# Optimization experiments

Hardware: AMD Instinct MI355X
Metric: run time of the kernel (lower is better)

## Reference

```python
import jax, jax.numpy as jnp
import numpy as np

B, N, D, H = 2, 2048, 1024, 16
DH = D // H            # 64
PH = 3 * DH            # 192 per-head proj dim (module quirk: 3*Dh per head)
P = H * PH             # 3072 total projection width


def setup_inputs() -> dict:
    key = jax.random.key(0)
    ks = jax.random.split(key, 8)
    s = 0.02
    return {
        "input": jax.random.normal(ks[0], (B, N, D), dtype=jnp.float32),
        "q_w": jax.random.normal(ks[1], (D, P), dtype=jnp.float32) * s,
        "q_b": jnp.zeros((P,), dtype=jnp.float32),
        "k_w": jax.random.normal(ks[2], (D, P), dtype=jnp.float32) * s,
        "k_b": jnp.zeros((P,), dtype=jnp.float32),
        "v_w": jax.random.normal(ks[3], (D, P), dtype=jnp.float32) * s,
        "v_b": jnp.zeros((P,), dtype=jnp.float32),
        "o_w": jax.random.normal(ks[4], (P, D), dtype=jnp.float32) * s,
        "o_b": jnp.zeros((D,), dtype=jnp.float32),
    }


def reference(input, q_w, q_b, k_w, k_b, v_w, v_b, o_w, o_b):
    def heads(y):  # [B,N,H*PH] -> [B,H,N,PH]
        return y.reshape(B, N, H, PH).transpose(0, 2, 1, 3)

    q_mat = heads(input @ q_w + q_b)
    # faithful to source: v_mat uses the 'k' projection, k_mat uses the 'v' projection
    v_mat = heads(input @ k_w + k_b)
    k_mat = heads(input @ v_w + v_b)

    scale = 1.0 / jnp.sqrt(jnp.float32(DH * H))  # sqrt(dim), per source
    scores = jnp.einsum('bhnd,bhmd->bhnm', q_mat, k_mat) * scale
    weights = jax.nn.softmax(scores, axis=-1)
    inter = jnp.einsum('bhnm,bhmd->bhnd', weights, v_mat)
    inter = inter.transpose(0, 2, 1, 3).reshape(B, N, P)  # b n (h d)
    return inter @ o_w + o_b
```

## Files before the change

### kernel.cpp

```cpp
#include <hip/hip_runtime.h>
#include <cstdint>
#include <cstddef>

typedef __bf16 bf16;
typedef __attribute__((ext_vector_type(8))) __bf16 bf16x8;
typedef __attribute__((ext_vector_type(4))) __bf16 bf16x4;
typedef __attribute__((ext_vector_type(2))) __bf16 bf16x2;
typedef __attribute__((ext_vector_type(4))) float f32x4;

#define MFMA_16x16x32(a, b, c) __builtin_amdgcn_mfma_f32_16x16x32_bf16((a), (b), (c), 0, 0, 0)

#define VMCNT(N) asm volatile("s_waitcnt vmcnt(" #N ")" ::: "memory")
#define LGK0                                           \
  {                                                    \
    asm volatile("s_waitcnt lgkmcnt(0)" ::: "memory"); \
    __builtin_amdgcn_sched_barrier(0);                 \
  }

__device__ __forceinline__ void gload_lds16(const void* g, void* l) {
  __builtin_amdgcn_global_load_lds((__attribute__((address_space(1))) void*)g,
                                   (__attribute__((address_space(3))) void*)l,
                                   16, 0, 0);
}

__global__ __launch_bounds__(256) void prep_kernel(const float* __restrict__ X,
                                                   const float* __restrict__ q_w,
                                                   const float* __restrict__ v_w,
                                                   const float* __restrict__ k_w,
                                                   const float* __restrict__ o_w,
                                                   bf16* __restrict__ Xb,
                                                   bf16* __restrict__ Wqkv,
                                                   bf16* __restrict__ Wot) {
  __shared__ float tile[32][33];
  int blk = blockIdx.x;
  if (blk < 4096) {
    int i = blk * 256 + threadIdx.x;
    float4 v = ((const float4*)X)[i];
    bf16x4 o = {(bf16)v.x, (bf16)v.y, (bf16)v.z, (bf16)v.w};
    ((bf16x4*)Xb)[i] = o;
    return;
  }
  const float* in;
  bf16* out;
  int R, C, t;
  if (blk < 13312) {
    t = blk - 4096;
    int widx = t / 3072;
    t -= widx * 3072;
    in = widx == 0 ? q_w : (widx == 1 ? v_w : k_w);
    out = Wqkv + (size_t)widx * 3072 * 1024;
    R = 1024;
    C = 3072;
  } else {
    t = blk - 13312;
    in = o_w;
    out = Wot;
    R = 3072;
    C = 1024;
  }
  int tiles_c = C >> 5;
  int br = t / tiles_c, bc = t % tiles_c;
  int r0 = br << 5, c0 = bc << 5;
  int tr = threadIdx.x >> 5, tc = threadIdx.x & 31;
#pragma unroll
  for (int i = 0; i < 4; i++)
    tile[tr + 8 * i][tc] = in[(size_t)(r0 + tr + 8 * i) * C + c0 + tc];
  __syncthreads();
#pragma unroll
  for (int i = 0; i < 4; i++) {
    int oc = tr + 8 * i;
    out[(size_t)(c0 + oc) * R + r0 + tc] = (bf16)tile[tc][oc];
  }
}

__global__ __launch_bounds__(512, 2) void gemm_fused_qkv(
    const bf16* __restrict__ A, const bf16* __restrict__ Bt,
    const float* __restrict__ q_b, const float* __restrict__ v_b,
    const float* __restrict__ k_b,
    bf16* __restrict__ Qm, bf16* __restrict__ Km, bf16* __restrict__ Vt) {
  constexpr int K = 1024, NT = 16;
  __shared__ __align__(16) bf16 sA[2][2][128 * 32];
  __shared__ __align__(16) bf16 sB[2][192 * 64];

  int bid = blockIdx.x;
  int xcd = bid & 7, j = bid >> 3;
  int bm = xcd * 4 + (j & 3), bn = j >> 2;
  int m0 = bm << 7, n0 = bn * 192;

  int tid = threadIdx.x, lane = tid & 63, w = tid >> 6;
  int wr = w >> 2, wc = w & 3;
  int l15 = lane & 15, lg = lane >> 4;

  int sra = lane >> 2, sca = lane & 3;
  const bf16* gA = A + (size_t)(m0 + w * 16 + sra) * K + ((sca ^ ((sra >> 1) & 3)) * 8);
  int srb = lane >> 3, scb = lane & 7;
  const bf16* gB = Bt + (size_t)(n0 + w * 24 + srb) * K + ((scb ^ srb) * 8);

#define STAGE_AB(BUF, T)                                                   \
  {                                                                        \
    _Pragma("unroll") for (int kh = 0; kh < 2; kh++)                       \
        gload_lds16(gA + (size_t)(T) * 64 + kh * 32, &sA[BUF][kh][w * 512]); \
    _Pragma("unroll") for (int ii = 0; ii < 3; ii++)                       \
        gload_lds16(gB + (size_t)(ii * 8) * K + (T) * 64,                  \
                    &sB[BUF][(w * 3 + ii) * 512]);                         \
  }

  int slotA = lg ^ ((l15 >> 1) & 3);
  int aBase = wr * 2048 + l15 * 32 + slotA * 8;
  int bBase = (wc * 48 + l15) * 64;
  int sB0 = (lg ^ (l15 & 7)) * 8;
  int sB1 = ((4 + lg) ^ (l15 & 7)) * 8;

#define RD_A(BUF, KH)                                                      \
  _Pragma("unroll") for (int mf = 0; mf < 4; mf++)                         \
      a[mf] = *(const bf16x8*)&sA[BUF][KH][aBase + mf * 512];
#define RD_B(BUF, SLOT)                                                    \
  _Pragma("unroll") for (int nf = 0; nf < 3; nf++)                         \
      b[nf] = *(const bf16x8*)&sB[BUF][bBase + nf * 1024 + (SLOT)];
#define MFMA12                                                             \
  _Pragma("unroll") for (int mf = 0; mf < 4; mf++)                         \
      _Pragma("unroll") for (int nf = 0; nf < 3; nf++)                     \
          acc[mf][nf] = MFMA_16x16x32(a[mf], b[nf], acc[mf][nf]);

  f32x4 acc[4][3];
#pragma unroll
  for (int mf = 0; mf < 4; mf++)
#pragma unroll
    for (int nf = 0; nf < 3; nf++) acc[mf][nf] = (f32x4){0.f, 0.f, 0.f, 0.f};

  STAGE_AB(0, 0);

#pragma unroll 2
  for (int s = 0; s < NT; s++) {
    int buf = s & 1, nbuf = buf ^ 1;
    int nxt = (s + 1) & (NT - 1);
    bf16x8 a[4], b[3];

    STAGE_AB(nbuf, nxt);
    VMCNT(5);
    __builtin_amdgcn_s_barrier();

    RD_A(buf, 0);
    RD_B(buf, sB0);
    LGK0;
    __builtin_amdgcn_s_setprio(1);
    MFMA12;
    __builtin_amdgcn_s_setprio(0);

    RD_A(buf, 1);
    RD_B(buf, sB1);
    LGK0;
    __builtin_amdgcn_s_barrier();
    __builtin_amdgcn_s_setprio(1);
    MFMA12;
    __builtin_amdgcn_s_setprio(0);
  }

  int seg = bn >> 4;
  int segbn = bn & 15;
  const float* bias = seg == 0 ? q_b : (seg == 1 ? v_b : k_b);
  bf16* outQK = seg == 0 ? Qm : Km;
#pragma unroll
  for (int mf = 0; mf < 4; mf++) {
#pragma unroll
    for (int nf = 0; nf < 3; nf++) {
      int colL = segbn * 192 + wc * 48 + nf * 16 + l15;
      int row0 = m0 + wr * 64 + mf * 16 + lg * 4;
      float bv = bias[colL];
      if (seg < 2) {
#pragma unroll
        for (int r = 0; r < 4; r++)
          outQK[(size_t)(row0 + r) * 3072 + colL] = (bf16)(acc[mf][nf][r] + bv);
      } else {
        int hh = colL / 192, dd = colL % 192;
        int bi = row0 >> 11, nn = row0 & 2047;
        bf16x4 pk = {(bf16)(acc[mf][nf][0] + bv), (bf16)(acc[mf][nf][1] + bv),
                     (bf16)(acc[mf][nf][2] + bv), (bf16)(acc[mf][nf][3] + bv)};
        *(bf16x4*)(Vt + (((size_t)bi * 16 + hh) * 192 + dd) * 2048 + nn) = pk;
      }
    }
  }
#undef STAGE_AB
#undef RD_A
#undef RD_B
#undef MFMA12
}

__global__ __launch_bounds__(256, 3) void gemm_oproj(const bf16* __restrict__ A,
                                                     const bf16* __restrict__ Bt,
                                                     const float* __restrict__ bias,
                                                     float* __restrict__ out) {
  constexpr int K = 3072, NT = 48;
  __shared__ __align__(16) bf16 sA[2][2][128 * 32];
  __shared__ __align__(16) bf16 sB[2][2][64 * 32];

  int bid = blockIdx.x;
  int xcd = bid & 7, j = bid >> 3;
  int bm = xcd * 4 + (j & 3), bn = j >> 2;
  int m0 = bm << 7, n0 = bn << 6;

  int tid = threadIdx.x, lane = tid & 63, w = tid >> 6;
  int wr = w >> 1, wc = w & 1;
  int l15 = lane & 15, lg = lane >> 4;

  int sra = lane >> 2, sca = lane & 3;
  int swzS = (sca ^ ((sra >> 1) & 3)) * 8;
  const bf16* gA = A + (size_t)(m0 + w * 32 + sra) * K + swzS;
  const bf16* gB = Bt + (size_t)(n0 + w * 16 + sra) * K + swzS;

#define O_STAGE(BUF, T)                                                     \
  {                                                                         \
    _Pragma("unroll") for (int kh = 0; kh < 2; kh++) {                      \
      _Pragma("unroll") for (int ii = 0; ii < 2; ii++)                      \
          gload_lds16(gA + (size_t)(ii * 16) * K + (T) * 64 + kh * 32,      \
                      &sA[BUF][kh][(w * 32 + ii * 16) * 32]);               \
      gload_lds16(gB + (size_t)(T) * 64 + kh * 32, &sB[BUF][kh][w * 512]);  \
    }                                                                       \
  }

  int slotA = lg ^ ((l15 >> 1) & 3);
  int aBase = (wr * 64 + l15) * 32 + slotA * 8;
  int bBase = (wc * 32 + l15) * 32 + slotA * 8;

#define O_RD(BUF, KH)                                                      \
  {                                                                        \
    _Pragma("unroll") for (int mf = 0; mf < 4; mf++)                       \
        a[mf] = *(const bf16x8*)&sA[BUF][KH][aBase + mf * 512];             \
    _Pragma("unroll") for (int nf = 0; nf < 2; nf++)                       \
        b[nf] = *(const bf16x8*)&sB[BUF][KH][bBase + nf * 512];             \
  }
#define O_MFMA8                                                            \
  _Pragma("unroll") for (int mf = 0; mf < 4; mf++)                         \
      _Pragma("unroll") for (int nf = 0; nf < 2; nf++)                     \
          acc[mf][nf] = MFMA_16x16x32(a[mf], b[nf], acc[mf][nf]);

  f32x4 acc[4][2];
#pragma unroll
  for (int mf = 0; mf < 4; mf++)
#pragma unroll
    for (int nf = 0; nf < 2; nf++) acc[mf][nf] = (f32x4){0.f, 0.f, 0.f, 0.f};

  O_STAGE(0, 0);

#pragma unroll 2
  for (int s = 0; s < NT; s++) {
    int buf = s & 1, nbuf = buf ^ 1;
    int nxt = s + 1 < NT ? s + 1 : 0;
    bf16x8 a[4], b[2];

    O_STAGE(nbuf, nxt);
    VMCNT(6);
    __builtin_amdgcn_s_barrier();

    O_RD(buf, 0);
    LGK0;
    __builtin_amdgcn_s_setprio(1);
    O_MFMA8;
    __builtin_amdgcn_s_setprio(0);

    O_RD(buf, 1);
    LGK0;
    __builtin_amdgcn_s_barrier();
    __builtin_amdgcn_s_setprio(1);
    O_MFMA8;
    __builtin_amdgcn_s_setprio(0);
  }

#pragma unroll
  for (int mf = 0; mf < 4; mf++) {
#pragma unroll
    for (int nf = 0; nf < 2; nf++) {
      int col = n0 + wc * 32 + nf * 16 + l15;
      int row0 = m0 + wr * 64 + mf * 16 + lg * 4;
      float bv = bias[col];
#pragma unroll
      for (int r = 0; r < 4; r++)
        out[(size_t)(row0 + r) * 1024 + col] = acc[mf][nf][r] + bv;
    }
  }
#undef O_STAGE
#undef O_RD
#undef O_MFMA8
}

__global__ __launch_bounds__(512, 2) void attn_kernel(const bf16* __restrict__ Q,
                                                      const bf16* __restrict__ Km,
                                                      const bf16* __restrict__ Vt,
                                                      bf16* __restrict__ inter) {
  __shared__ __align__(16) bf16 sK[2][32 * 192];
  __shared__ __align__(16) bf16 sV[2][192 * 32];
  __shared__ __align__(16) bf16 sPT[8 * 16 * 40];

  int i = blockIdx.x;
  int j = i >> 3;
  int bh = (i & 7) * 4 + (j >> 4);
  int qt = j & 15;
  int b = bh >> 4, h = bh & 15;
  int tid = threadIdx.x, lane = tid & 63, w = tid >> 6;
  int l15 = lane & 15, lg = lane >> 4;
  int swz = l15 & 7;

  const bf16* Qh = Q + (size_t)b * 2048 * 3072 + (size_t)h * 192;
  const bf16* Kh = Km + (size_t)b * 2048 * 3072 + (size_t)h * 192;
  const bf16* Vh = Vt + (size_t)bh * 192 * 2048;

  int q0 = qt * 128 + w * 16;

  const bf16* gsrc[3];
  int gstride[3];
  bf16* lbase[3];
#pragma unroll
  for (int ii = 0; ii < 3; ii++) {
    int g = ii * 512 + tid;
    if (g < 768) {
      int krow = g / 24, kc = g % 24;
      int kcs = (kc & 24) | ((kc & 7) ^ (krow & 7));
      gsrc[ii] = Kh + krow * 3072 + kcs * 8;
      gstride[ii] = 32 * 3072;
      lbase[ii] = &sK[0][g * 8];
    } else {
      int gg = g - 768;
      int vrow = gg >> 2, vc = gg & 3;
      int vcs = vc ^ ((vrow >> 1) & 3);
      gsrc[ii] = Vh + vrow * 2048 + vcs * 8;
      gstride[ii] = 32;
      lbase[ii] = &sV[0][gg * 8];
    }
  }

#define STAGE(BUF, KT)                                                      \
  {                                                                         \
    _Pragma("unroll") for (int ii = 0; ii < 3; ii++)                        \
        gload_lds16(gsrc[ii] + (size_t)(KT) * gstride[ii],                  \
                    lbase[ii] + (BUF) * 6144);                              \
  }

  STAGE(0, 0);

  bf16x8 aq[6];
#pragma unroll
  for (int kc = 0; kc < 6; kc++)
    aq[kc] = *(const bf16x8*)(Qh + (size_t)(q0 + l15) * 3072 + kc * 32 + lg * 8);

  f32x4 o[12];
#pragma unroll
  for (int df = 0; df < 12; df++) o[df] = (f32x4){0.f, 0.f, 0.f, 0.f};
  float lsum = 0.f;

  const float scl2 = 0.03125f * 1.44269504f;

  bf16* myPT = &sPT[(w * 16 + l15) * 40];
  int cv = lg ^ ((l15 >> 1) & 3);

  __syncthreads();

  for (int kt = 0; kt < 64; kt++) {
    const bf16* kbuf = sK[kt & 1];
    const bf16* vbuf = sV[kt & 1];
    if (kt < 63) STAGE((kt & 1) ^ 1, kt + 1);

    f32x4 st[2];
    st[0] = (f32x4){0.f, 0.f, 0.f, 0.f};
    st[1] = (f32x4){0.f, 0.f, 0.f, 0.f};
    __builtin_amdgcn_s_setprio(1);
#pragma unroll
    for (int kc = 0; kc < 6; kc++) {
      int g = kc * 4 + lg;
      int cc = (g & 24) | ((g & 7) ^ swz);
#pragma unroll
      for (int kf = 0; kf < 2; kf++) {
        bf16x8 bk = *(const bf16x8*)&kbuf[(kf * 16 + l15) * 192 + cc * 8];
        st[kf] = MFMA_16x16x32(bk, aq[kc], st[kf]);
      }
    }
    __builtin_amdgcn_s_setprio(0);

#pragma unroll
    for (int kf = 0; kf < 2; kf++) {
      float e0 = exp2f(st[kf][0] * scl2);
      float e1 = exp2f(st[kf][1] * scl2);
      float e2 = exp2f(st[kf][2] * scl2);
      float e3 = exp2f(st[kf][3] * scl2);
      lsum += (e0 + e1) + (e2 + e3);
      bf16x4 pk4 = {(bf16)e0, (bf16)e1, (bf16)e2, (bf16)e3};
      *(bf16x4*)&myPT[kf * 16 + 4 * lg] = pk4;
    }

    bf16x8 pf = *(const bf16x8*)&myPT[lg * 8];

    __builtin_amdgcn_s_setprio(1);
#pragma unroll
    for (int df = 0; df < 12; df++) {
      bf16x8 av = *(const bf16x8*)&vbuf[(df * 16 + l15) * 32 + cv * 8];
      o[df] = MFMA_16x16x32(av, pf, o[df]);
    }
    __builtin_amdgcn_s_setprio(0);

    __syncthreads();
  }

  {
    lsum += __shfl_xor(lsum, 16);
    lsum += __shfl_xor(lsum, 32);
    float inv = 1.0f / lsum;
    size_t token = (size_t)b * 2048 + q0 + l15;
    bf16* outp = inter + token * 3072 + h * 192 + lg * 4;
#pragma unroll
    for (int df = 0; df < 12; df++) {
      bf16x4 pk = {(bf16)(o[df][0] * inv), (bf16)(o[df][1] * inv),
                   (bf16)(o[df][2] * inv), (bf16)(o[df][3] * inv)};
      *(bf16x4*)(outp + df * 16) = pk;
    }
  }
#undef STAGE
}

extern "C" void kernel_launch(void* const* d_in, const int* in_sizes, int n_in,
                              void* d_out, int out_size, void* d_ws, size_t ws_size,
                              hipStream_t stream) {
  const float* X = (const float*)d_in[0];
  const float* q_w = (const float*)d_in[1];
  const float* q_b = (const float*)d_in[2];
  const float* k_w = (const float*)d_in[3];
  const float* k_b = (const float*)d_in[4];
  const float* v_w = (const float*)d_in[5];
  const float* v_b = (const float*)d_in[6];
  const float* o_w = (const float*)d_in[7];
  const float* o_b = (const float*)d_in[8];

  char* ws = (char*)d_ws;
  bf16* Xb  = (bf16*)(ws);
  bf16* Wqt = (bf16*)(ws + 8388608);
  bf16* Wot = (bf16*)(ws + 27262976);
  bf16* Qm  = (bf16*)(ws + 33554432);
  bf16* Km  = (bf16*)(ws + 58720256);
  bf16* Vtw = (bf16*)(ws + 83886080);
  bf16* Im  = (bf16*)(ws + 109051904);

  prep_kernel<<<16384, 256, 0, stream>>>(X, q_w, v_w, k_w, o_w, Xb, Wqt, Wot);

  gemm_fused_qkv<<<1536, 512, 0, stream>>>(Xb, Wqt, q_b, v_b, k_b, Qm, Km, Vtw);

  attn_kernel<<<512, 512, 0, stream>>>(Qm, Km, Vtw, Im);

  gemm_oproj<<<512, 256, 0, stream>>>(Im, Wot, o_b, (float*)d_out);
}
```

Before: 258.8 us.

## Keep softmax probabilities in registers by permuting V layout; prescale Q

The attention kernel no longer round-trips exponentiated scores through LDS to rebuild the MFMA B operand. The scores are packed straight from registers, and the V-transpose store in the QKV GEMM permutes the key index within each 32-key block so the register order lines up with the V operand. The softmax scale times log2(e) is folded into the Q epilogue before rounding to bf16, which removes per-element multiplies in the loop. Folding the scale into Q before the bf16 cast slightly changes rounding, and correctness now depends on the permutation matching the fragment layout exactly.

```diff
diff --git a/kernel.cpp b/kernel.cpp
--- a/kernel.cpp
+++ b/kernel.cpp
@@ -21,6 +21,11 @@
   __builtin_amdgcn_global_load_lds((__attribute__((address_space(1))) void*)g,
                                    (__attribute__((address_space(3))) void*)l,
                                    16, 0, 0);
+}
+
+__device__ __forceinline__ uint32_t pack2(float a, float b) {
+  bf16x2 h = {(bf16)a, (bf16)b};
+  return __builtin_bit_cast(uint32_t, h);
 }
 
 __global__ __launch_bounds__(256) void prep_kernel(const float* __restrict__ X,
@@ -156,6 +161,7 @@
     __builtin_amdgcn_s_setprio(0);
   }
 
+  const float scl2 = 0.03125f * 1.44269504f;
   int seg = bn >> 4;
   int segbn = bn & 15;
   const float* bias = seg == 0 ? q_b : (seg == 1 ? v_b : k_b);
@@ -167,16 +173,22 @@
       int colL = segbn * 192 + wc * 48 + nf * 16 + l15;
       int row0 = m0 + wr * 64 + mf * 16 + lg * 4;
       float bv = bias[colL];
-      if (seg < 2) {
+      if (seg == 0) {
+#pragma unroll
+        for (int r = 0; r < 4; r++)
+          outQK[(size_t)(row0 + r) * 3072 + colL] = (bf16)((acc[mf][nf][r] + bv) * scl2);
+      } else if (seg == 1) {
 #pragma unroll
         for (int r = 0; r < 4; r++)
           outQK[(size_t)(row0 + r) * 3072 + colL] = (bf16)(acc[mf][nf][r] + bv);
       } else {
         int hh = colL / 192, dd = colL % 192;
         int bi = row0 >> 11, nn = row0 & 2047;
+        int jj = (nn >> 2) & 7;
+        int nnp = (nn & ~31) | ((jj & 3) << 3) | ((jj >> 2) << 2);
         bf16x4 pk = {(bf16)(acc[mf][nf][0] + bv), (bf16)(acc[mf][nf][1] + bv),
                      (bf16)(acc[mf][nf][2] + bv), (bf16)(acc[mf][nf][3] + bv)};
-        *(bf16x4*)(Vt + (((size_t)bi * 16 + hh) * 192 + dd) * 2048 + nn) = pk;
+        *(bf16x4*)(Vt + (((size_t)bi * 16 + hh) * 192 + dd) * 2048 + nnp) = pk;
       }
     }
   }
@@ -289,7 +301,6 @@
                                                       bf16* __restrict__ inter) {
   __shared__ __align__(16) bf16 sK[2][32 * 192];
   __shared__ __align__(16) bf16 sV[2][192 * 32];
-  __shared__ __align__(16) bf16 sPT[8 * 16 * 40];
 
   int i = blockIdx.x;
   int j = i >> 3;
@@ -347,9 +358,6 @@
   for (int df = 0; df < 12; df++) o[df] = (f32x4){0.f, 0.f, 0.f, 0.f};
   float lsum = 0.f;
 
-  const float scl2 = 0.03125f * 1.44269504f;
-
-  bf16* myPT = &sPT[(w * 16 + l15) * 40];
   int cv = lg ^ ((l15 >> 1) & 3);
 
   __syncthreads();
@@ -375,18 +383,17 @@
     }
     __builtin_amdgcn_s_setprio(0);
 
-#pragma unroll
-    for (int kf = 0; kf < 2; kf++) {
-      float e0 = exp2f(st[kf][0] * scl2);
-      float e1 = exp2f(st[kf][1] * scl2);
-      float e2 = exp2f(st[kf][2] * scl2);
-      float e3 = exp2f(st[kf][3] * scl2);
-      lsum += (e0 + e1) + (e2 + e3);
-      bf16x4 pk4 = {(bf16)e0, (bf16)e1, (bf16)e2, (bf16)e3};
-      *(bf16x4*)&myPT[kf * 16 + 4 * lg] = pk4;
-    }
-
-    bf16x8 pf = *(const bf16x8*)&myPT[lg * 8];
+    float e00 = exp2f(st[0][0]), e01 = exp2f(st[0][1]);
+    float e02 = exp2f(st[0][2]), e03 = exp2f(st[0][3]);
+    float e10 = exp2f(st[1][0]), e11 = exp2f(st[1][1]);
+    float e12 = exp2f(st[1][2]), e13 = exp2f(st[1][3]);
+    lsum += ((e00 + e01) + (e02 + e03)) + ((e10 + e11) + (e12 + e13));
+    union { uint32_t u[4]; bf16x8 v; } fb;
+    fb.u[0] = pack2(e00, e01);
+    fb.u[1] = pack2(e02, e03);
+    fb.u[2] = pack2(e10, e11);
+    fb.u[3] = pack2(e12, e13);
+    bf16x8 pf = fb.v;
 
     __builtin_amdgcn_s_setprio(1);
 #pragma unroll
```

New measurement: 254.7 us. No clear change (-1.6%).
